# Kernel tuning notes

Measured on AMD Instinct MI355X. Metric: run time of the kernel, lower is better.

Reference implementation:

```python
import jax, jax.numpy as jnp
import numpy as np

EPS = 1e-6  # torch CosineSimilarity eps
L = 2


def _norm0(a):
    # L2 norm along hidden axis (axis 0), clamped at eps like torch cosine_similarity
    return jnp.maximum(jnp.sqrt(jnp.sum(a * a, axis=0)), EPS)


def _cos_pair(a, b):
    # a, b: (H, B, S) -> (B, S), cosine along hidden dim
    return jnp.sum(a * b, axis=0) / (_norm0(a) * _norm0(b))


def _cos_cross(a, b):
    # a: (H, B, I), b: (H, B, J) -> (B, I, J) pairwise cosine along hidden dim
    num = jnp.einsum('hbi,hbj->bij', a, b)
    return num / (_norm0(a)[:, :, None] * _norm0(b)[:, None, :])


def _persp(wv1, wv2, wv3, wv4, p, q):
    # wv*: (H,) perspective weight vectors; p: (H,B,SP); q: (H,B,SQ)
    # --- m1: full matching vs last timestep of q ---
    w1 = wv1[:, None, None]
    wp1 = w1 * p                      # (H,B,SP)
    wq_last = wv1[:, None] * q[:, :, -1]  # (H,B)
    nq = jnp.maximum(jnp.sqrt(jnp.sum(wq_last * wq_last, axis=0)), EPS)  # (B,)
    m1 = jnp.einsum('hbs,hb->bs', wp1, wq_last) / (_norm0(wp1) * nq[:, None])
    # --- m2: maxpool matching over all q positions (weighted) ---
    w2 = wv2[:, None, None]
    m2 = jnp.max(_cos_cross(w2 * p, w2 * q), axis=2)  # (B,SP)
    # --- shared unweighted pairwise cosine attention (B,SP,SQ) ---
    att = _cos_cross(p, q)
    # --- m3: attentive matching (mean-attended q) ---
    attn = att / jnp.sum(att, axis=2, keepdims=True)
    hmean = jnp.einsum('bij,hbj->hbi', attn, q)  # (H,B,SP)
    w3 = wv3[:, None, None]
    m3 = _cos_pair(w3 * p, w3 * hmean)
    # --- m4: max-attentive matching (gather argmax q position) ---
    idx = jnp.argmax(att, axis=2)  # (B,SP)
    hmax = jnp.take_along_axis(q, jnp.broadcast_to(idx[None], (q.shape[0],) + idx.shape), axis=2)
    w4 = wv4[:, None, None]
    m4 = _cos_pair(w4 * p, w4 * hmax)
    return m1, m2, m3, m4


def setup_inputs() -> dict:
    key = jax.random.key(0)
    ks = jax.random.split(key, 12)
    H, B, SP, SQ = 100, 64, 384, 384
    mk = lambda k, s: jax.random.normal(k, s, dtype=jnp.float32)
    return {
        'p_f': mk(ks[0], (H, B, SP)), 'p_b': mk(ks[1], (H, B, SP)),
        'q_f': mk(ks[2], (H, B, SQ)), 'q_b': mk(ks[3], (H, B, SQ)),
        'w1f': mk(ks[4], (L, H)), 'w1b': mk(ks[5], (L, H)),
        'w2f': mk(ks[6], (L, H)), 'w2b': mk(ks[7], (L, H)),
        'w3f': mk(ks[8], (L, H)), 'w3b': mk(ks[9], (L, H)),
        'w4f': mk(ks[10], (L, H)), 'w4b': mk(ks[11], (L, H)),
    }


def reference(p_f, p_b, q_f, q_b, w1f, w1b, w2f, w2b, w3f, w3b, w4f, w4b):
    acc = [[] for _ in range(8)]  # m1f,m1b,m2f,m2b,m3f,m3b,m4f,m4b
    for l in range(L):
        # forward direction
        f1, f2, f3, f4 = _persp(w1f[l], w2f[l], w3f[l], w4f[l], p_f, q_f)
        # backward direction; NOTE: original code (bug preserved) uses the
        # *forward* tables match_w_3_f / match_w_4_f for backward m3/m4.
        b1, b2, b3, b4 = _persp(w1b[l], w2b[l], w3f[l], w4f[l], p_b, q_b)
        for i, s in enumerate([f1, b1, f2, b2, f3, b3, f4, b4]):
            acc[i].append(s.T)  # (SP, B), matching sim.permute(1,0)
    ms = tuple(jnp.stack(a, axis=2) for a in acc)  # each (SP, B, L)
    return ms
```

## Files before the change

### kernel.cpp

```cpp
#include <hip/hip_runtime.h>
#include <math.h>

#define HH 100
#define HP 112
#define KP 136
#define BB 64
#define SS 384
#define EPSF 1e-6f
#define NCH 24
#define QT16 4352
#define QT_PITCH_B 9216
#define QHJ_OFF_B 18432
#define QHJ_ROWP 40
#define BNC_OFF_B 27392
#define BNCP 36
#define STATB_OFF_B 29696
#define SMEM_B 36608

typedef __attribute__((ext_vector_type(8))) short bf16x8;
typedef __attribute__((ext_vector_type(4))) float f32x4;
typedef unsigned short ushort_t;

__device__ __forceinline__ ushort_t f2bf(float x) {
  unsigned u = __float_as_uint(x);
  unsigned r = (u + 0x7FFFu + ((u >> 16) & 1u)) >> 16;
  return (ushort_t)r;
}
__device__ __forceinline__ float bf2f(ushort_t h) {
  return __uint_as_float(((unsigned)h) << 16);
}
__device__ __forceinline__ void ld_g2l16(void* lds, const void* g) {
  __builtin_amdgcn_global_load_lds(
      (const __attribute__((address_space(1))) unsigned*)g,
      (__attribute__((address_space(3))) unsigned*)lds, 16, 0, 0);
}

__global__ __launch_bounds__(256) void qprep_kernel(
    const float* __restrict__ qf, const float* __restrict__ qb,
    const float* __restrict__ w2f, const float* __restrict__ w2b,
    float* __restrict__ nq2, ushort_t* __restrict__ qhj_hi,
    ushort_t* __restrict__ qTil)
{
  __shared__ __align__(16) float tile[HH * 68];
  __shared__ float w2sq_s[HH][2];
  const int blk = blockIdx.x;
  const int dir = blk / (BB * 6);
  const int rem = blk % (BB * 6);
  const int b   = rem / 6;
  const int jt  = rem % 6;
  const int j0  = jt * 64;
  const float* q  = dir ? qb : qf;
  const float* w2 = dir ? w2b : w2f;
  const int t = threadIdx.x;
  if (t < HH) {
    float a = w2[t], c = w2[HH + t];
    w2sq_s[t][0] = a * a; w2sq_s[t][1] = c * c;
  }
  for (int e = t; e < HH * 16; e += 256) {
    int h = e >> 4, j4 = e & 15;
    float4 v = *(const float4*)&q[((size_t)h * BB + b) * SS + j0 + j4 * 4];
    *(float4*)&tile[h * 68 + j4 * 4] = v;
  }
  __syncthreads();
  for (int e = t; e < 64 * KP; e += 256) {
    int jj = e / KP, kp = e % KP;
    float x = (kp < HH) ? tile[kp * 68 + jj] : 0.f;
    ushort_t hi = f2bf(x);
    int cg = jt * 4 + (jj >> 4);
    size_t base = ((size_t)(dir * BB + b) * NCH + cg) * QT16
                + (size_t)(jj & 15) * KP + kp;
    qTil[base] = hi;
    qTil[base + 16 * KP] = f2bf(x - bf2f(hi));
  }
  for (int e = t; e < HP * 64; e += 256) {
    int hp = e >> 6, jj = e & 63;
    float x = (hp < HH) ? tile[hp * 68 + jj] : 0.f;
    size_t o = ((size_t)(dir * HP + hp) * BB + b) * SS + j0 + jj;
    qhj_hi[o] = f2bf(x);
  }
  if (t < 64) {
    float s0 = 0.f, s1 = 0.f, sp = 0.f;
    for (int h = 0; h < HH; ++h) {
      float v = tile[h * 68 + t];
      float v2 = v * v;
      s0 = fmaf(w2sq_s[h][0], v2, s0);
      s1 = fmaf(w2sq_s[h][1], v2, s1);
      sp += v2;
    }
    int j = j0 + t;
    nq2[((size_t)(dir * 2 + 0) * BB + b) * SS + j] = 1.0f / fmaxf(sqrtf(s0), EPSF);
    nq2[((size_t)(dir * 2 + 1) * BB + b) * SS + j] = 1.0f / fmaxf(sqrtf(s1), EPSF);
    nq2[((size_t)(4 + dir) * BB + b) * SS + j]     = 1.0f / fmaxf(sqrtf(sp), EPSF);
  }
}

__global__ __launch_bounds__(256, 3) void bimpm_fused(
    const float* __restrict__ pf, const float* __restrict__ pb,
    const float* __restrict__ qf, const float* __restrict__ qb,
    const float* __restrict__ w1f, const float* __restrict__ w1b,
    const float* __restrict__ w2f, const float* __restrict__ w2b,
    const float* __restrict__ w3f_, const float* __restrict__ w4f_,
    const float* __restrict__ nq2ws,
    const ushort_t* __restrict__ qhj_hi, const ushort_t* __restrict__ qTil,
    float* __restrict__ out)
{
  __shared__ __align__(16) char smemc[SMEM_B];
  __shared__ __align__(16) float wsq[HH][8];
  __shared__ float qlast_s[HH];

  float* hmbuf = (float*)smemc;
  float* statb = (float*)(smemc + STATB_OFF_B);
  float* bounce = (float*)(smemc + BNC_OFF_B);

  const int bid  = blockIdx.x;
  const int work = (bid & 7) * 96 + (bid >> 3);
  const int dir = work / (BB * 6);
  const int rem = work % (BB * 6);
  const int b   = rem / 6;
  const int i0  = (rem % 6) * 64;

  const float* __restrict__ p  = dir ? pb : pf;
  const float* __restrict__ q  = dir ? qb : qf;
  const float* __restrict__ w1 = dir ? w1b : w1f;
  const float* __restrict__ w2 = dir ? w2b : w2f;
  const int t = threadIdx.x;
  const int w = t >> 6, lane = t & 63, li = lane & 15, lg = lane >> 4;
  const int rowbase = i0 + w * 16;
  const size_t AS = (size_t)SS * BB * 2;
  const size_t qt_base = (size_t)(dir * BB + b) * NCH * QT16;
  const ushort_t* __restrict__ qhjH0 = qhj_hi + ((size_t)dir * HP * BB + b) * SS;

  if (t < HH) {
    float a, c;
    a = w1[t];   c = w1[HH + t];   wsq[t][0] = a*a; wsq[t][1] = c*c;
    a = w2[t];   c = w2[HH + t];   wsq[t][2] = a*a; wsq[t][3] = c*c;
    a = w3f_[t]; c = w3f_[HH + t]; wsq[t][4] = a*a; wsq[t][5] = c*c;
    a = w4f_[t]; c = w4f_[HH + t]; wsq[t][6] = a*a; wsq[t][7] = c*c;
    qlast_s[t] = q[(size_t)t * BB * SS + (size_t)b * SS + (SS - 1)];
  }

  auto stage_qt = [&](int cc, int bi) {
    char* dst = smemc + bi * QT_PITCH_B;
    const char* gsrc = (const char*)(qTil + qt_base + (size_t)cc * QT16);
#pragma unroll
    for (int k = 0; k < 2; ++k) {
      const int sb = k * 256 + w * 64;
      ld_g2l16(dst + (size_t)sb * 16, gsrc + (size_t)(sb + lane) * 16);
    }
    if (w == 0 && lane < 32)
      ld_g2l16(dst + (size_t)512 * 16, gsrc + (size_t)(512 + lane) * 16);
  };
  auto stage_qhj = [&](int P) {
    char* dst = smemc + QHJ_OFF_B;
#pragma unroll
    for (int k = 0; k < 3; ++k) {
      const int sb = k * 256 + w * 64;
      if (k < 2 || (w == 0 && lane < 48)) {
        int v = sb + lane;
        int hp = v / 5;
        int s = v - hp * 5;
        if (s == 4) s = 0;
        const ushort_t* src = qhjH0 + (size_t)hp * (BB * SS) + P * 32 + s * 8;
        ld_g2l16(dst + (size_t)sb * 16, src);
      }
    }
  };

  stage_qt(0, 0);
  stage_qhj(0);

  bf16x8 pHi[4], pLo[4], pGa[4], pGb[4];
#pragma unroll
  for (int kt = 0; kt < 4; ++kt) {
#pragma unroll
    for (int s = 0; s < 8; ++s) {
      int h = kt * 32 + 8 * lg + s;
      float pv = 0.f, ga = 0.f, gb = 0.f;
      if (h < HH) {
        pv = p[(size_t)h * BB * SS + (size_t)b * SS + rowbase + li];
        float wa = w2[h], wb = w2[HH + h];
        ga = pv * wa * wa;
        gb = pv * wb * wb;
      }
      ushort_t hi = f2bf(pv);
      pHi[kt][s] = (short)hi;
      pLo[kt][s] = (short)f2bf(pv - bf2f(hi));
      pGa[kt][s] = (short)f2bf(ga);
      pGb[kt][s] = (short)f2bf(gb);
    }
  }
  __syncthreads();

  f32x4 hmD[7];
#pragma unroll
  for (int nt = 0; nt < 7; ++nt) hmD[nt] = (f32x4){0.f, 0.f, 0.f, 0.f};
  float rowsum[4] = {0, 0, 0, 0};
  float amax[4] = {-INFINITY, -INFINITY, -INFINITY, -INFINITY};
  float m2a[4] = {-INFINITY, -INFINITY, -INFINITY, -INFINITY};
  float m2b[4] = {-INFINITY, -INFINITY, -INFINITY, -INFINITY};
  int aidx[4] = {0, 0, 0, 0};
  const float* nqa = nq2ws + ((size_t)(dir * 2 + 0) * BB + b) * SS;
  const float* nqb = nq2ws + ((size_t)(dir * 2 + 1) * BB + b) * SS;
  const float* nqp = nq2ws + ((size_t)(4 + dir) * BB + b) * SS;
  float* bw = bounce + w * (16 * BNCP);
  const ushort_t* qjR = (const ushort_t*)(smemc + QHJ_OFF_B);

  for (int c = 0; c < NCH; ++c) {
    const bool evenc = (c & 1) == 0;
    if (c + 1 < NCH) stage_qt(c + 1, (c + 1) & 1);
    if (evenc && c > 0) stage_qhj(c >> 1);

    const ushort_t* bufc = (const ushort_t*)(smemc + (c & 1) * QT_PITCH_B);
    const ushort_t* qtH = bufc;
    const ushort_t* qtL = bufc + 16 * KP;

    f32x4 attD = {0, 0, 0, 0}, gaD = {0, 0, 0, 0}, gbD = {0, 0, 0, 0};
#pragma unroll
    for (int kt = 0; kt < 4; ++kt) {
      const int bo = li * KP + kt * 32 + 8 * lg;
      bf16x8 bHi = *(const bf16x8*)&qtH[bo];
      bf16x8 bLo = *(const bf16x8*)&qtL[bo];
      attD = __builtin_amdgcn_mfma_f32_16x16x32_bf16(pHi[kt], bHi, attD, 0, 0, 0);
      attD = __builtin_amdgcn_mfma_f32_16x16x32_bf16(pLo[kt], bHi, attD, 0, 0, 0);
      attD = __builtin_amdgcn_mfma_f32_16x16x32_bf16(pHi[kt], bLo, attD, 0, 0, 0);
      gaD  = __builtin_amdgcn_mfma_f32_16x16x32_bf16(pGa[kt], bHi, gaD, 0, 0, 0);
      gbD  = __builtin_amdgcn_mfma_f32_16x16x32_bf16(pGb[kt], bHi, gbD, 0, 0, 0);
    }
    {
      const int j = c * 16 + li;
      const float rp = nqp[j], ra = nqa[j], rb = nqb[j];
#pragma unroll
      for (int r = 0; r < 4; ++r) {
        float d = attD[r] * rp;
        rowsum[r] += d;
        if (d > amax[r]) { amax[r] = d; aidx[r] = j; }
        m2a[r] = fmaxf(m2a[r], gaD[r] * ra);
        m2b[r] = fmaxf(m2b[r], gbD[r] * rb);
        bw[(lg * 4 + r) * BNCP + (c & 1) * 16 + li] = d;
      }
    }
    if (!evenc) {
      asm volatile("s_waitcnt lgkmcnt(0)" ::: "memory");
      __builtin_amdgcn_sched_barrier(0);
      float4 v0 = *(const float4*)&bw[li * BNCP + lg * 8];
      float4 v1 = *(const float4*)&bw[li * BNCP + lg * 8 + 4];
      union { bf16x8 v; unsigned u[4]; } Hd, Ld;
      {
        float xf[8] = {v0.x, v0.y, v0.z, v0.w, v1.x, v1.y, v1.z, v1.w};
#pragma unroll
        for (int pr = 0; pr < 4; ++pr) {
          unsigned u0 = __float_as_uint(xf[2 * pr]);
          unsigned u1 = __float_as_uint(xf[2 * pr + 1]);
          Hd.u[pr] = (u0 >> 16) | (u1 & 0xFFFF0000u);
          float r0 = xf[2 * pr]     - __uint_as_float(u0 & 0xFFFF0000u);
          float r1 = xf[2 * pr + 1] - __uint_as_float(u1 & 0xFFFF0000u);
          Ld.u[pr] = (__float_as_uint(r0) >> 16) | (__float_as_uint(r1) & 0xFFFF0000u);
        }
      }
#pragma unroll
      for (int nt = 0; nt < 7; ++nt) {
        const int ro = (nt * 16 + li) * QHJ_ROWP + lg * 8;
        bf16x8 qHi = *(const bf16x8*)&qjR[ro];
        hmD[nt] = __builtin_amdgcn_mfma_f32_16x16x32_bf16(Hd.v, qHi, hmD[nt], 0, 0, 0);
        hmD[nt] = __builtin_amdgcn_mfma_f32_16x16x32_bf16(Ld.v, qHi, hmD[nt], 0, 0, 0);
      }
    }
    __syncthreads();
  }

#pragma unroll
  for (int r = 0; r < 4; ++r) {
#pragma unroll
    for (int m = 1; m < 16; m <<= 1) {
      rowsum[r] += __shfl_xor(rowsum[r], m);
      float ov = __shfl_xor(amax[r], m);
      int   oi = __shfl_xor(aidx[r], m);
      if (ov > amax[r] || (ov == amax[r] && oi < aidx[r])) { amax[r] = ov; aidx[r] = oi; }
      m2a[r] = fmaxf(m2a[r], __shfl_xor(m2a[r], m));
      m2b[r] = fmaxf(m2b[r], __shfl_xor(m2b[r], m));
    }
  }
  if (li == 0) {
#pragma unroll
    for (int r = 0; r < 4; ++r) {
      const int row = lg * 4 + r;
      statb[((w * 16) + row) * 4 + 0] = (rowsum[r] < 0.f) ? -1.f : 1.f;
      statb[((w * 16) + row) * 4 + 1] = __int_as_float(aidx[r]);
      statb[((w * 16) + row) * 4 + 2] = m2a[r];
      statb[((w * 16) + row) * 4 + 3] = m2b[r];
    }
  }
#pragma unroll
  for (int nt = 0; nt < 7; ++nt) {
#pragma unroll
    for (int r = 0; r < 4; ++r) {
      hmbuf[(size_t)(w * 16 + lg * 4 + r) * 116 + nt * 16 + li] = hmD[nt][r];
    }
  }
  __syncthreads();

  {
    const int row = lane & 15, hq = lane >> 4;
    const int gi = rowbase + row;
    const float sg   = statb[((w * 16) + row) * 4 + 0];
    const int   ax   = __float_as_int(statb[((w * 16) + row) * 4 + 1]);
    const float m2av = statb[((w * 16) + row) * 4 + 2];
    const float m2bv = statb[((w * 16) + row) * 4 + 3];
    float ps0=0,ps1=0,ps2=0,ps3=0,ps4=0,ps5=0,ps6=0,ps7=0;
    float m1n0=0,m1n1=0,nq1a=0,nq1b=0;
    float m3n0=0,m3n1=0,nh0=0,nh1=0;
    float m4n0=0,m4n1=0,nq4a=0,nq4b=0;
#pragma unroll 5
    for (int k = 0; k < 25; ++k) {
      int h = k * 4 + hq;
      float pv = p[(size_t)h * BB * SS + (size_t)b * SS + gi];
      float hm = hmbuf[(size_t)(w * 16 + row) * 116 + h];
      float ql = qlast_s[h];
      float qi = q[(size_t)h * BB * SS + (size_t)b * SS + ax];
      float4 wv0 = *(const float4*)&wsq[h][0];
      float4 wv1 = *(const float4*)&wsq[h][4];
      float p2 = pv * pv;
      ps0 = fmaf(wv0.x, p2, ps0); ps1 = fmaf(wv0.y, p2, ps1);
      ps2 = fmaf(wv0.z, p2, ps2); ps3 = fmaf(wv0.w, p2, ps3);
      ps4 = fmaf(wv1.x, p2, ps4); ps5 = fmaf(wv1.y, p2, ps5);
      ps6 = fmaf(wv1.z, p2, ps6); ps7 = fmaf(wv1.w, p2, ps7);
      m1n0 = fmaf(wv0.x, pv * ql, m1n0); m1n1 = fmaf(wv0.y, pv * ql, m1n1);
      nq1a = fmaf(wv0.x, ql * ql, nq1a); nq1b = fmaf(wv0.y, ql * ql, nq1b);
      m3n0 = fmaf(wv1.x, pv * hm, m3n0); m3n1 = fmaf(wv1.y, pv * hm, m3n1);
      nh0  = fmaf(wv1.x, hm * hm, nh0);  nh1  = fmaf(wv1.y, hm * hm, nh1);
      m4n0 = fmaf(wv1.z, pv * qi, m4n0); m4n1 = fmaf(wv1.w, pv * qi, m4n1);
      nq4a = fmaf(wv1.z, qi * qi, nq4a); nq4b = fmaf(wv1.w, qi * qi, nq4b);
    }
#pragma unroll
    for (int m = 16; m < 64; m <<= 1) {
      ps0 += __shfl_xor(ps0, m);  ps1 += __shfl_xor(ps1, m);
      ps2 += __shfl_xor(ps2, m);  ps3 += __shfl_xor(ps3, m);
      ps4 += __shfl_xor(ps4, m);  ps5 += __shfl_xor(ps5, m);
      ps6 += __shfl_xor(ps6, m);  ps7 += __shfl_xor(ps7, m);
      m1n0 += __shfl_xor(m1n0, m); m1n1 += __shfl_xor(m1n1, m);
      nq1a += __shfl_xor(nq1a, m); nq1b += __shfl_xor(nq1b, m);
      m3n0 += __shfl_xor(m3n0, m); m3n1 += __shfl_xor(m3n1, m);
      nh0  += __shfl_xor(nh0,  m); nh1  += __shfl_xor(nh1,  m);
      m4n0 += __shfl_xor(m4n0, m); m4n1 += __shfl_xor(m4n1, m);
      nq4a += __shfl_xor(nq4a, m); nq4b += __shfl_xor(nq4b, m);
    }
    if (hq == 0) {
      const size_t base = (size_t)gi * (BB * 2) + (size_t)b * 2;
      out[(size_t)(0 + dir) * AS + base + 0] =
          m1n0 / (fmaxf(sqrtf(ps0), EPSF) * fmaxf(sqrtf(nq1a), EPSF));
      out[(size_t)(0 + dir) * AS + base + 1] =
          m1n1 / (fmaxf(sqrtf(ps1), EPSF) * fmaxf(sqrtf(nq1b), EPSF));
      out[(size_t)(2 + dir) * AS + base + 0] = m2av / fmaxf(sqrtf(ps2), EPSF);
      out[(size_t)(2 + dir) * AS + base + 1] = m2bv / fmaxf(sqrtf(ps3), EPSF);
      out[(size_t)(4 + dir) * AS + base + 0] =
          sg * m3n0 / (fmaxf(sqrtf(ps4), EPSF) * fmaxf(sqrtf(nh0), EPSF));
      out[(size_t)(4 + dir) * AS + base + 1] =
          sg * m3n1 / (fmaxf(sqrtf(ps5), EPSF) * fmaxf(sqrtf(nh1), EPSF));
      out[(size_t)(6 + dir) * AS + base + 0] =
          m4n0 / (fmaxf(sqrtf(ps6), EPSF) * fmaxf(sqrtf(nq4a), EPSF));
      out[(size_t)(6 + dir) * AS + base + 1] =
          m4n1 / (fmaxf(sqrtf(ps7), EPSF) * fmaxf(sqrtf(nq4b), EPSF));
    }
  }
}

extern "C" void kernel_launch(void* const* d_in, const int* in_sizes, int n_in,
                              void* d_out, int out_size, void* d_ws, size_t ws_size,
                              hipStream_t stream) {
  const float* pf  = (const float*)d_in[0];
  const float* pb  = (const float*)d_in[1];
  const float* qf  = (const float*)d_in[2];
  const float* qb  = (const float*)d_in[3];
  const float* w1f = (const float*)d_in[4];
  const float* w1b = (const float*)d_in[5];
  const float* w2f = (const float*)d_in[6];
  const float* w2b = (const float*)d_in[7];
  const float* w3f = (const float*)d_in[8];
  const float* w4f = (const float*)d_in[10];
  float* out = (float*)d_out;

  const size_t nq2_b  = (size_t)6 * BB * SS * 4;
  const size_t qhj_b  = (size_t)2 * HP * BB * SS * 2;
  float*    nq2    = (float*)d_ws;
  ushort_t* qhj_hi = (ushort_t*)((char*)d_ws + nq2_b);
  ushort_t* qTil   = (ushort_t*)((char*)d_ws + nq2_b + qhj_b);

  hipLaunchKernelGGL(qprep_kernel, dim3(2 * BB * 6), dim3(256), 0, stream,
                     qf, qb, w2f, w2b, nq2, qhj_hi, qTil);
  hipLaunchKernelGGL(bimpm_fused, dim3(2 * BB * 6), dim3(256), 0, stream,
                     pf, pb, qf, qb, w1f, w1b, w2f, w2b, w3f, w4f,
                     nq2, qhj_hi, qTil, out);
}
```

Baseline: 74.19 us.

## Fuse q-prep and main kernel via cooperative grid sync; split attention accumulator

Merges the q preprocessing kernel and the main matching kernel into one cooperative launch, with a grid-wide sync between the prep phase and the main phase. The goal is to remove the second kernel launch and the gap between kernels. If the cooperative launch fails, it falls back to the old two-kernel path. It also splits the attention MFMA accumulator into two independent chains over even and odd k-tiles to shorten the dependency chain. The costs are a grid barrier, a residency requirement of 768 blocks co-resident at 3 per CU, and possible extra register pressure from the fused body.

```diff
diff --git a/kernel.cpp b/kernel.cpp
--- a/kernel.cpp
+++ b/kernel.cpp
@@ -1,4 +1,5 @@
 #include <hip/hip_runtime.h>
+#include <hip/hip_cooperative_groups.h>
 #include <math.h>
 
 #define HH 100
@@ -21,6 +22,8 @@
 typedef __attribute__((ext_vector_type(4))) float f32x4;
 typedef unsigned short ushort_t;
 
+namespace cg = cooperative_groups;
+
 __device__ __forceinline__ ushort_t f2bf(float x) {
   unsigned u = __float_as_uint(x);
   unsigned r = (u + 0x7FFFu + ((u >> 16) & 1u)) >> 16;
@@ -35,26 +38,21 @@
       (__attribute__((address_space(3))) unsigned*)lds, 16, 0, 0);
 }
 
-__global__ __launch_bounds__(256) void qprep_kernel(
+__device__ __forceinline__ void prep_body(
+    int dir, int b, int jt,
     const float* __restrict__ qf, const float* __restrict__ qb,
     const float* __restrict__ w2f, const float* __restrict__ w2b,
     float* __restrict__ nq2, ushort_t* __restrict__ qhj_hi,
-    ushort_t* __restrict__ qTil)
+    ushort_t* __restrict__ qTil, char* smem, int t)
 {
-  __shared__ __align__(16) float tile[HH * 68];
-  __shared__ float w2sq_s[HH][2];
-  const int blk = blockIdx.x;
-  const int dir = blk / (BB * 6);
-  const int rem = blk % (BB * 6);
-  const int b   = rem / 6;
-  const int jt  = rem % 6;
-  const int j0  = jt * 64;
+  float* tile = (float*)smem;
+  float* w2sq = (float*)(smem + 27200);
+  const int j0 = jt * 64;
   const float* q  = dir ? qb : qf;
   const float* w2 = dir ? w2b : w2f;
-  const int t = threadIdx.x;
   if (t < HH) {
     float a = w2[t], c = w2[HH + t];
-    w2sq_s[t][0] = a * a; w2sq_s[t][1] = c * c;
+    w2sq[t * 2] = a * a; w2sq[t * 2 + 1] = c * c;
   }
   for (int e = t; e < HH * 16; e += 256) {
     int h = e >> 4, j4 = e & 15;
@@ -66,8 +64,8 @@
     int jj = e / KP, kp = e % KP;
     float x = (kp < HH) ? tile[kp * 68 + jj] : 0.f;
     ushort_t hi = f2bf(x);
-    int cg = jt * 4 + (jj >> 4);
-    size_t base = ((size_t)(dir * BB + b) * NCH + cg) * QT16
+    int cg_ = jt * 4 + (jj >> 4);
+    size_t base = ((size_t)(dir * BB + b) * NCH + cg_) * QT16
                 + (size_t)(jj & 15) * KP + kp;
     qTil[base] = hi;
     qTil[base + 16 * KP] = f2bf(x - bf2f(hi));
@@ -83,8 +81,8 @@
     for (int h = 0; h < HH; ++h) {
       float v = tile[h * 68 + t];
       float v2 = v * v;
-      s0 = fmaf(w2sq_s[h][0], v2, s0);
-      s1 = fmaf(w2sq_s[h][1], v2, s1);
+      s0 = fmaf(w2sq[h * 2], v2, s0);
+      s1 = fmaf(w2sq[h * 2 + 1], v2, s1);
       sp += v2;
     }
     int j = j0 + t;
@@ -94,7 +92,8 @@
   }
 }
 
-__global__ __launch_bounds__(256, 3) void bimpm_fused(
+__device__ __forceinline__ void main_body(
+    int dir, int b, int i0,
     const float* __restrict__ pf, const float* __restrict__ pb,
     const float* __restrict__ qf, const float* __restrict__ qb,
     const float* __restrict__ w1f, const float* __restrict__ w1b,
@@ -102,28 +101,16 @@
     const float* __restrict__ w3f_, const float* __restrict__ w4f_,
     const float* __restrict__ nq2ws,
     const ushort_t* __restrict__ qhj_hi, const ushort_t* __restrict__ qTil,
-    float* __restrict__ out)
+    float* __restrict__ out, char* smemc, float* wsq, float* qlast_s, int t)
 {
-  __shared__ __align__(16) char smemc[SMEM_B];
-  __shared__ __align__(16) float wsq[HH][8];
-  __shared__ float qlast_s[HH];
-
   float* hmbuf = (float*)smemc;
   float* statb = (float*)(smemc + STATB_OFF_B);
   float* bounce = (float*)(smemc + BNC_OFF_B);
-
-  const int bid  = blockIdx.x;
-  const int work = (bid & 7) * 96 + (bid >> 3);
-  const int dir = work / (BB * 6);
-  const int rem = work % (BB * 6);
-  const int b   = rem / 6;
-  const int i0  = (rem % 6) * 64;
 
   const float* __restrict__ p  = dir ? pb : pf;
   const float* __restrict__ q  = dir ? qb : qf;
   const float* __restrict__ w1 = dir ? w1b : w1f;
   const float* __restrict__ w2 = dir ? w2b : w2f;
-  const int t = threadIdx.x;
   const int w = t >> 6, lane = t & 63, li = lane & 15, lg = lane >> 4;
   const int rowbase = i0 + w * 16;
   const size_t AS = (size_t)SS * BB * 2;
@@ -132,10 +119,10 @@
 
   if (t < HH) {
     float a, c;
-    a = w1[t];   c = w1[HH + t];   wsq[t][0] = a*a; wsq[t][1] = c*c;
-    a = w2[t];   c = w2[HH + t];   wsq[t][2] = a*a; wsq[t][3] = c*c;
-    a = w3f_[t]; c = w3f_[HH + t]; wsq[t][4] = a*a; wsq[t][5] = c*c;
-    a = w4f_[t]; c = w4f_[HH + t]; wsq[t][6] = a*a; wsq[t][7] = c*c;
+    a = w1[t];   c = w1[HH + t];   wsq[t*8+0] = a*a; wsq[t*8+1] = c*c;
+    a = w2[t];   c = w2[HH + t];   wsq[t*8+2] = a*a; wsq[t*8+3] = c*c;
+    a = w3f_[t]; c = w3f_[HH + t]; wsq[t*8+4] = a*a; wsq[t*8+5] = c*c;
+    a = w4f_[t]; c = w4f_[HH + t]; wsq[t*8+6] = a*a; wsq[t*8+7] = c*c;
     qlast_s[t] = q[(size_t)t * BB * SS + (size_t)b * SS + (SS - 1)];
   }
 
@@ -214,24 +201,31 @@
     const ushort_t* qtH = bufc;
     const ushort_t* qtL = bufc + 16 * KP;
 
-    f32x4 attD = {0, 0, 0, 0}, gaD = {0, 0, 0, 0}, gbD = {0, 0, 0, 0};
+    f32x4 attD0 = {0, 0, 0, 0}, attD1 = {0, 0, 0, 0};
+    f32x4 gaD = {0, 0, 0, 0}, gbD = {0, 0, 0, 0};
 #pragma unroll
     for (int kt = 0; kt < 4; ++kt) {
       const int bo = li * KP + kt * 32 + 8 * lg;
       bf16x8 bHi = *(const bf16x8*)&qtH[bo];
       bf16x8 bLo = *(const bf16x8*)&qtL[bo];
-      attD = __builtin_amdgcn_mfma_f32_16x16x32_bf16(pHi[kt], bHi, attD, 0, 0, 0);
-      attD = __builtin_amdgcn_mfma_f32_16x16x32_bf16(pLo[kt], bHi, attD, 0, 0, 0);
-      attD = __builtin_amdgcn_mfma_f32_16x16x32_bf16(pHi[kt], bLo, attD, 0, 0, 0);
-      gaD  = __builtin_amdgcn_mfma_f32_16x16x32_bf16(pGa[kt], bHi, gaD, 0, 0, 0);
-      gbD  = __builtin_amdgcn_mfma_f32_16x16x32_bf16(pGb[kt], bHi, gbD, 0, 0, 0);
+      if ((kt & 1) == 0) {
+        attD0 = __builtin_amdgcn_mfma_f32_16x16x32_bf16(pHi[kt], bHi, attD0, 0, 0, 0);
+        attD0 = __builtin_amdgcn_mfma_f32_16x16x32_bf16(pLo[kt], bHi, attD0, 0, 0, 0);
+        attD0 = __builtin_amdgcn_mfma_f32_16x16x32_bf16(pHi[kt], bLo, attD0, 0, 0, 0);
+      } else {
+        attD1 = __builtin_amdgcn_mfma_f32_16x16x32_bf16(pHi[kt], bHi, attD1, 0, 0, 0);
+        attD1 = __builtin_amdgcn_mfma_f32_16x16x32_bf16(pLo[kt], bHi, attD1, 0, 0, 0);
+        attD1 = __builtin_amdgcn_mfma_f32_16x16x32_bf16(pHi[kt], bLo, attD1, 0, 0, 0);
+      }
+      gaD = __builtin_amdgcn_mfma_f32_16x16x32_bf16(pGa[kt], bHi, gaD, 0, 0, 0);
+      gbD = __builtin_amdgcn_mfma_f32_16x16x32_bf16(pGb[kt], bHi, gbD, 0, 0, 0);
     }
     {
       const int j = c * 16 + li;
       const float rp = nqp[j], ra = nqa[j], rb = nqb[j];
 #pragma unroll
       for (int r = 0; r < 4; ++r) {
-        float d = attD[r] * rp;
+        float d = (attD0[r] + attD1[r]) * rp;
         rowsum[r] += d;
         if (d > amax[r]) { amax[r] = d; aidx[r] = j; }
         m2a[r] = fmaxf(m2a[r], gaD[r] * ra);
@@ -317,8 +311,8 @@
       float hm = hmbuf[(size_t)(w * 16 + row) * 116 + h];
       float ql = qlast_s[h];
       float qi = q[(size_t)h * BB * SS + (size_t)b * SS + ax];
-      float4 wv0 = *(const float4*)&wsq[h][0];
-      float4 wv1 = *(const float4*)&wsq[h][4];
+      float4 wv0 = *(const float4*)&wsq[h * 8];
+      float4 wv1 = *(const float4*)&wsq[h * 8 + 4];
       float p2 = pv * pv;
       ps0 = fmaf(wv0.x, p2, ps0); ps1 = fmaf(wv0.y, p2, ps1);
       ps2 = fmaf(wv0.z, p2, ps2); ps3 = fmaf(wv0.w, p2, ps3);
@@ -364,6 +358,68 @@
   }
 }
 
+__global__ __launch_bounds__(256, 3) void bimpm_all(
+    const float* __restrict__ pf, const float* __restrict__ pb,
+    const float* __restrict__ qf, const float* __restrict__ qb,
+    const float* __restrict__ w1f, const float* __restrict__ w1b,
+    const float* __restrict__ w2f, const float* __restrict__ w2b,
+    const float* __restrict__ w3f_, const float* __restrict__ w4f_,
+    float* __restrict__ nq2, ushort_t* __restrict__ qhj_hi,
+    ushort_t* __restrict__ qTil, float* __restrict__ out)
+{
+  __shared__ __align__(16) char smemc[SMEM_B];
+  __shared__ __align__(16) float wsq[HH * 8];
+  __shared__ float qlast_s[HH];
+  const int bid  = blockIdx.x;
+  const int work = (bid & 7) * 96 + (bid >> 3);
+  const int dir = work / (BB * 6);
+  const int rem = work % (BB * 6);
+  const int b   = rem / 6;
+  const int six = rem % 6;
+  const int t = threadIdx.x;
+
+  prep_body(dir, b, six, qf, qb, w2f, w2b, nq2, qhj_hi, qTil, smemc, t);
+  cg::this_grid().sync();
+  main_body(dir, b, six * 64, pf, pb, qf, qb, w1f, w1b, w2f, w2b, w3f_, w4f_,
+            nq2, qhj_hi, qTil, out, smemc, wsq, qlast_s, t);
+}
+
+__global__ __launch_bounds__(256) void qprep_kernel(
+    const float* __restrict__ qf, const float* __restrict__ qb,
+    const float* __restrict__ w2f, const float* __restrict__ w2b,
+    float* __restrict__ nq2, ushort_t* __restrict__ qhj_hi,
+    ushort_t* __restrict__ qTil)
+{
+  __shared__ __align__(16) char smem[28000];
+  const int blk = blockIdx.x;
+  const int dir = blk / (BB * 6);
+  const int rem = blk % (BB * 6);
+  prep_body(dir, rem / 6, rem % 6, qf, qb, w2f, w2b, nq2, qhj_hi, qTil,
+            smem, threadIdx.x);
+}
+
+__global__ __launch_bounds__(256, 3) void bimpm_fused(
+    const float* __restrict__ pf, const float* __restrict__ pb,
+    const float* __restrict__ qf, const float* __restrict__ qb,
+    const float* __restrict__ w1f, const float* __restrict__ w1b,
+    const float* __restrict__ w2f, const float* __restrict__ w2b,
+    const float* __restrict__ w3f_, const float* __restrict__ w4f_,
+    const float* __restrict__ nq2ws,
+    const ushort_t* __restrict__ qhj_hi, const ushort_t* __restrict__ qTil,
+    float* __restrict__ out)
+{
+  __shared__ __align__(16) char smemc[SMEM_B];
+  __shared__ __align__(16) float wsq[HH * 8];
+  __shared__ float qlast_s[HH];
+  const int bid  = blockIdx.x;
+  const int work = (bid & 7) * 96 + (bid >> 3);
+  const int dir = work / (BB * 6);
+  const int rem = work % (BB * 6);
+  main_body(dir, rem / 6, (rem % 6) * 64, pf, pb, qf, qb, w1f, w1b, w2f, w2b,
+            w3f_, w4f_, nq2ws, qhj_hi, qTil, out, smemc, wsq, qlast_s,
+            threadIdx.x);
+}
+
 extern "C" void kernel_launch(void* const* d_in, const int* in_sizes, int n_in,
                               void* d_out, int out_size, void* d_ws, size_t ws_size,
                               hipStream_t stream) {
@@ -385,9 +441,15 @@
   ushort_t* qhj_hi = (ushort_t*)((char*)d_ws + nq2_b);
   ushort_t* qTil   = (ushort_t*)((char*)d_ws + nq2_b + qhj_b);
 
-  hipLaunchKernelGGL(qprep_kernel, dim3(2 * BB * 6), dim3(256), 0, stream,
-                     qf, qb, w2f, w2b, nq2, qhj_hi, qTil);
-  hipLaunchKernelGGL(bimpm_fused, dim3(2 * BB * 6), dim3(256), 0, stream,
-                     pf, pb, qf, qb, w1f, w1b, w2f, w2b, w3f, w4f,
-                     nq2, qhj_hi, qTil, out);
-}
+  void* args[] = {&pf, &pb, &qf, &qb, &w1f, &w1b, &w2f, &w2b, &w3f, &w4f,
+                  &nq2, &qhj_hi, &qTil, &out};
+  hipError_t err = hipLaunchCooperativeKernel(
+      (void*)bimpm_all, dim3(2 * BB * 6), dim3(256), args, 0, stream);
+  if (err != hipSuccess) {
+    hipLaunchKernelGGL(qprep_kernel, dim3(2 * BB * 6), dim3(256), 0, stream,
+                       qf, qb, w2f, w2b, nq2, qhj_hi, qTil);
+    hipLaunchKernelGGL(bimpm_fused, dim3(2 * BB * 6), dim3(256), 0, stream,
+                       pf, pb, qf, qb, w1f, w1b, w2f, w2b, w3f, w4f,
+                       nq2, qhj_hi, qTil, out);
+  }
+}
```

New measurement: 127.0 us. +71.2%, slower.
